# Optimization experiments

Hardware: AMD Instinct MI355X
Metric: run time of the kernel (lower is better)

## Reference

```python
import jax, jax.numpy as jnp
import numpy as np

TAU = 0.08


def setup_inputs() -> dict:
    key = jax.random.key(0)
    k1, k2 = jax.random.split(key)
    pos_waves = jax.random.normal(k1, (32, 64, 8192), dtype=jnp.float32)
    neg_waves = jax.random.normal(k2, (32, 64, 8192), dtype=jnp.float32)
    return {"pos_waves": pos_waves, "neg_waves": neg_waves}


def _normalize(w):
    # global min/max over the whole wave tensor (matches torch.min/torch.max on 2D tensor)
    lo = jnp.min(w, axis=(1, 2), keepdims=True)  # [N,1,1]
    hi = jnp.max(w, axis=(1, 2), keepdims=True)
    return (w - lo) / (hi - lo)


def _pairwise_negpearson(X, Y):
    # X: [N,B,T], Y: [M,B,T] -> mean over B of (1 - pearson) for every (n,m) pair
    T = X.shape[-1]
    sx = jnp.sum(X, axis=-1)            # [N,B]
    sy = jnp.sum(Y, axis=-1)            # [M,B]
    sx2 = jnp.sum(X * X, axis=-1)       # [N,B]
    sy2 = jnp.sum(Y * Y, axis=-1)       # [M,B]
    sxy = jnp.einsum('nbt,mbt->nmb', X, Y)  # [N,M,B]
    num = T * sxy - sx[:, None, :] * sy[None, :, :]
    den = jnp.sqrt((T * sx2 - sx * sx)[:, None, :] * (T * sy2 - sy * sy)[None, :, :])
    return jnp.mean(1.0 - num / den, axis=-1)  # [N,M]


def reference(pos_waves, neg_waves):
    P = _normalize(pos_waves)   # [N,B,T]
    Q = _normalize(neg_waves)   # [M,B,T]
    N = P.shape[0]

    d_pp = _pairwise_negpearson(P, P)                    # [N,N]
    upper = jnp.triu(jnp.ones((N, N), dtype=bool), k=1)  # i < j pairs only
    pos_total = jnp.sum(jnp.where(upper, jnp.exp(d_pp / TAU), 0.0))

    d_pn = _pairwise_negpearson(P, Q)                    # [N,M]
    neg_total = jnp.sum(jnp.exp(d_pn / TAU))

    return jnp.log10(pos_total / neg_total + 1.0)
```

## Files before the change

### kernel.cpp

```cpp
#include <hip/hip_runtime.h>
#include <cmath>

#define N_ 32
#define B_ 64
#define T_ 8192
#define NBLK1 1024
#define PS 2176

typedef _Float16 half8 __attribute__((ext_vector_type(8)));
typedef float floatx4 __attribute__((ext_vector_type(4)));

__device__ __forceinline__ half8 cvt8(const float4 v0, const float4 v1,
                                      float& s, float& s2) {
    s += v0.x + v0.y + v0.z + v0.w + v1.x + v1.y + v1.z + v1.w;
    s2 = fmaf(v0.x, v0.x, s2); s2 = fmaf(v0.y, v0.y, s2);
    s2 = fmaf(v0.z, v0.z, s2); s2 = fmaf(v0.w, v0.w, s2);
    s2 = fmaf(v1.x, v1.x, s2); s2 = fmaf(v1.y, v1.y, s2);
    s2 = fmaf(v1.z, v1.z, s2); s2 = fmaf(v1.w, v1.w, s2);
    half8 r = {(_Float16)v0.x, (_Float16)v0.y, (_Float16)v0.z, (_Float16)v0.w,
               (_Float16)v1.x, (_Float16)v1.y, (_Float16)v1.z, (_Float16)v1.w};
    return r;
}

__global__ __launch_bounds__(256, 2)
void k_stage1(const float* __restrict__ pos, const float* __restrict__ neg,
              float* __restrict__ pt, double* __restrict__ accs,
              unsigned* __restrict__ ctr) {
    __shared__ float red_s[PS];
    const int bid = blockIdx.x;
    const int b = bid & 63, cg = bid >> 6;
    const int tid = threadIdx.x;
    const int w = tid >> 6, lane = tid & 63;
    const int m = lane & 15, h = lane >> 4;

    if (bid == 0 && tid == 0) { accs[0] = 0.0; accs[1] = 0.0; *ctr = 0u; }

    const long tb = (long)cg * 512 + w * 128 + h * 8;
    const float4* pa0 = (const float4*)(pos + ((long)m * B_ + b) * T_ + tb);
    const float4* pa1 = (const float4*)(pos + ((long)(m + 16) * B_ + b) * T_ + tb);
    const float4* pb0 = (const float4*)(neg + ((long)m * B_ + b) * T_ + tb);
    const float4* pb1 = (const float4*)(neg + ((long)(m + 16) * B_ + b) * T_ + tb);

    float4 a0[4][2], a1[4][2], b0[4][2], b1[4][2];
#pragma unroll
    for (int kk = 0; kk < 4; ++kk) {
        a0[kk][0] = pa0[kk * 8]; a0[kk][1] = pa0[kk * 8 + 1];
        a1[kk][0] = pa1[kk * 8]; a1[kk][1] = pa1[kk * 8 + 1];
        b0[kk][0] = pb0[kk * 8]; b0[kk][1] = pb0[kk * 8 + 1];
        b1[kk][0] = pb1[kk * 8]; b1[kk][1] = pb1[kk * 8 + 1];
    }

    floatx4 cPP00 = {}, cPP01 = {}, cPP11 = {};
    floatx4 cPN00 = {}, cPN01 = {}, cPN10 = {}, cPN11 = {};
    float sxl = 0.f, sxl2 = 0.f, sxh = 0.f, sxh2 = 0.f;
    float syl = 0.f, syl2 = 0.f, syh = 0.f, syh2 = 0.f;

#pragma unroll
    for (int kk = 0; kk < 4; ++kk) {
        half8 fa0 = cvt8(a0[kk][0], a0[kk][1], sxl, sxl2);
        half8 fa1 = cvt8(a1[kk][0], a1[kk][1], sxh, sxh2);
        half8 fb0 = cvt8(b0[kk][0], b0[kk][1], syl, syl2);
        half8 fb1 = cvt8(b1[kk][0], b1[kk][1], syh, syh2);
        cPP00 = __builtin_amdgcn_mfma_f32_16x16x32_f16(fa0, fa0, cPP00, 0, 0, 0);
        cPP01 = __builtin_amdgcn_mfma_f32_16x16x32_f16(fa0, fa1, cPP01, 0, 0, 0);
        cPP11 = __builtin_amdgcn_mfma_f32_16x16x32_f16(fa1, fa1, cPP11, 0, 0, 0);
        cPN00 = __builtin_amdgcn_mfma_f32_16x16x32_f16(fa0, fb0, cPN00, 0, 0, 0);
        cPN01 = __builtin_amdgcn_mfma_f32_16x16x32_f16(fa0, fb1, cPN01, 0, 0, 0);
        cPN10 = __builtin_amdgcn_mfma_f32_16x16x32_f16(fa1, fb0, cPN10, 0, 0, 0);
        cPN11 = __builtin_amdgcn_mfma_f32_16x16x32_f16(fa1, fb1, cPN11, 0, 0, 0);
    }

    sxl += __shfl_xor(sxl, 16);   sxl += __shfl_xor(sxl, 32);
    sxl2 += __shfl_xor(sxl2, 16); sxl2 += __shfl_xor(sxl2, 32);
    sxh += __shfl_xor(sxh, 16);   sxh += __shfl_xor(sxh, 32);
    sxh2 += __shfl_xor(sxh2, 16); sxh2 += __shfl_xor(sxh2, 32);
    syl += __shfl_xor(syl, 16);   syl += __shfl_xor(syl, 32);
    syl2 += __shfl_xor(syl2, 16); syl2 += __shfl_xor(syl2, 32);
    syh += __shfl_xor(syh, 16);   syh += __shfl_xor(syh, 32);
    syh2 += __shfl_xor(syh2, 16); syh2 += __shfl_xor(syh2, 32);

    for (int i = tid; i < PS; i += 256) red_s[i] = 0.f;
    __syncthreads();
#pragma unroll
    for (int wv = 0; wv < 4; ++wv) {
        if (w == wv) {
#pragma unroll
            for (int reg = 0; reg < 4; ++reg) {
                const int r = h * 4 + reg;
                red_s[r * 32 + m]                    += cPP00[reg];
                red_s[r * 32 + 16 + m]               += cPP01[reg];
                red_s[(16 + r) * 32 + 16 + m]        += cPP11[reg];
                red_s[1024 + r * 32 + m]             += cPN00[reg];
                red_s[1024 + r * 32 + 16 + m]        += cPN01[reg];
                red_s[1024 + (16 + r) * 32 + m]      += cPN10[reg];
                red_s[1024 + (16 + r) * 32 + 16 + m] += cPN11[reg];
            }
            const int row = (h & 1) * 16 + m;
            const int base = 2048 + (h >> 1) * 64;
            const float s1 = (h == 0) ? sxl : (h == 1) ? sxh : (h == 2) ? syl : syh;
            const float s2 = (h == 0) ? sxl2 : (h == 1) ? sxh2 : (h == 2) ? syl2 : syh2;
            red_s[base + row] += s1;
            red_s[base + 32 + row] += s2;
        }
        __syncthreads();
    }

    for (int i = tid; i < PS; i += 256)
        pt[(long)i * NBLK1 + bid] = red_s[i];
}

__global__ __launch_bounds__(256)
void k_entries(const float* __restrict__ pt, double* __restrict__ accs,
               unsigned* __restrict__ ctr, float* __restrict__ out) {
    const int tid = threadIdx.x;
    const int w = tid >> 6, lane = tid & 63;
    const int entry = blockIdx.x * 4 + w;
    const int mat = entry >> 10;
    const int idx = entry & 1023;
    const int n = idx >> 5, m = idx & 31;

    auto rowsum = [&](int o) -> float {
        const float* p = pt + (long)o * NBLK1 + lane;
        float s = 0.f;
#pragma unroll
        for (int c = 0; c < 16; ++c) s += p[c * 64];
        return s;
    };

    const float g    = rowsum(mat * 1024 + idx);
    const float sxn  = rowsum(2048 + n);
    const float sx2n = rowsum(2080 + n);
    const float sym  = rowsum(mat ? 2112 + m : 2048 + m);
    const float sy2m = rowsum(mat ? 2144 + m : 2080 + m);

    double num = (double)T_ * (double)g - (double)sxn * (double)sym;
    double vx = (double)T_ * (double)sx2n - (double)sxn * (double)sxn;
    double vy = (double)T_ * (double)sy2m - (double)sym * (double)sym;
    double contrib = 1.0 - num / sqrt(vx * vy);

#pragma unroll
    for (int off = 32; off; off >>= 1) contrib += __shfl_down(contrib, off);

    __shared__ double s_pos[4], s_neg[4];
    if (lane == 0) {
        double d = contrib * (1.0 / B_);
        double term = exp(d / 0.08);
        double p = 0.0, q = 0.0;
        if (mat == 0) { if (n < m) p = term; }
        else q = term;
        s_pos[w] = p; s_neg[w] = q;
    }
    __syncthreads();
    if (tid == 0) {
        atomicAdd(&accs[0], s_pos[0] + s_pos[1] + s_pos[2] + s_pos[3]);
        atomicAdd(&accs[1], s_neg[0] + s_neg[1] + s_neg[2] + s_neg[3]);
        __threadfence();
        const unsigned old = atomicAdd(ctr, 1u);
        if (old == gridDim.x - 1) {
            __threadfence();
            const double p = ((volatile double*)accs)[0];
            const double q = ((volatile double*)accs)[1];
            out[0] = (float)log10(p / q + 1.0);
        }
    }
}

extern "C" void kernel_launch(void* const* d_in, const int* in_sizes, int n_in,
                              void* d_out, int out_size, void* d_ws, size_t ws_size,
                              hipStream_t stream) {
    (void)in_sizes; (void)n_in; (void)out_size; (void)ws_size;
    const float* pos = (const float*)d_in[0];
    const float* neg = (const float*)d_in[1];
    float* out = (float*)d_out;

    char* ws = (char*)d_ws;
    float* pt = (float*)ws;
    double* accs = (double*)(ws + (size_t)PS * NBLK1 * 4);
    unsigned* ctr = (unsigned*)(ws + (size_t)PS * NBLK1 * 4 + 16);

    k_stage1<<<NBLK1, 256, 0, stream>>>(pos, neg, pt, accs, ctr);
    k_entries<<<512, 256, 0, stream>>>(pt, accs, ctr, out);
}
```

Baseline: 189.6 us.

## Write block partials contiguously and add a separate reduction kernel

Stage 1 now stores each block's partial sums as one contiguous row using float4 stores, replacing the previous transposed layout where every element went to a strided address. A new k_reduce kernel sums the 16 chunk partials for each batch index with coalesced reads. k_entries then reads the already-reduced values instead of summing 16 partials itself. The aim is to remove uncoalesced scattered writes from stage 1, at the cost of an extra kernel launch and an extra pass over the partial buffer.

```diff
diff --git a/kernel.cpp b/kernel.cpp
--- a/kernel.cpp
+++ b/kernel.cpp
@@ -24,9 +24,9 @@
 
 __global__ __launch_bounds__(256, 2)
 void k_stage1(const float* __restrict__ pos, const float* __restrict__ neg,
-              float* __restrict__ pt, double* __restrict__ accs,
+              float* __restrict__ partial, double* __restrict__ accs,
               unsigned* __restrict__ ctr) {
-    __shared__ float red_s[PS];
+    __shared__ __align__(16) float red_s[PS];
     const int bid = blockIdx.x;
     const int b = bid & 63, cg = bid >> 6;
     const int tid = threadIdx.x;
@@ -105,12 +105,22 @@
         __syncthreads();
     }
 
-    for (int i = tid; i < PS; i += 256)
-        pt[(long)i * NBLK1 + bid] = red_s[i];
+    const float4* rs = (const float4*)red_s;
+    float4* op = (float4*)(partial + (long)bid * PS);
+    for (int i = tid; i < PS / 4; i += 256) op[i] = rs[i];
+}
+
+__global__ void k_reduce(const float* __restrict__ partial, float* __restrict__ red) {
+    const int b = blockIdx.y;
+    const int o = blockIdx.x * 128 + threadIdx.x;
+    float s = 0.f;
+#pragma unroll
+    for (int c = 0; c < 16; ++c) s += partial[(long)(c * 64 + b) * PS + o];
+    red[(long)b * PS + o] = s;
 }
 
 __global__ __launch_bounds__(256)
-void k_entries(const float* __restrict__ pt, double* __restrict__ accs,
+void k_entries(const float* __restrict__ red, double* __restrict__ accs,
                unsigned* __restrict__ ctr, float* __restrict__ out) {
     const int tid = threadIdx.x;
     const int w = tid >> 6, lane = tid & 63;
@@ -119,19 +129,12 @@
     const int idx = entry & 1023;
     const int n = idx >> 5, m = idx & 31;
 
-    auto rowsum = [&](int o) -> float {
-        const float* p = pt + (long)o * NBLK1 + lane;
-        float s = 0.f;
-#pragma unroll
-        for (int c = 0; c < 16; ++c) s += p[c * 64];
-        return s;
-    };
-
-    const float g    = rowsum(mat * 1024 + idx);
-    const float sxn  = rowsum(2048 + n);
-    const float sx2n = rowsum(2080 + n);
-    const float sym  = rowsum(mat ? 2112 + m : 2048 + m);
-    const float sy2m = rowsum(mat ? 2144 + m : 2080 + m);
+    const float* rb = red + (long)lane * PS;
+    const float g    = rb[mat * 1024 + idx];
+    const float sxn  = rb[2048 + n];
+    const float sx2n = rb[2080 + n];
+    const float sym  = rb[mat ? 2112 + m : 2048 + m];
+    const float sy2m = rb[mat ? 2144 + m : 2080 + m];
 
     double num = (double)T_ * (double)g - (double)sxn * (double)sym;
     double vx = (double)T_ * (double)sx2n - (double)sxn * (double)sxn;
@@ -174,10 +177,12 @@
     float* out = (float*)d_out;
 
     char* ws = (char*)d_ws;
-    float* pt = (float*)ws;
-    double* accs = (double*)(ws + (size_t)PS * NBLK1 * 4);
-    unsigned* ctr = (unsigned*)(ws + (size_t)PS * NBLK1 * 4 + 16);
+    float* partial = (float*)ws;
+    float* red = (float*)(ws + (size_t)NBLK1 * PS * 4);
+    double* accs = (double*)(ws + (size_t)NBLK1 * PS * 4 + (size_t)64 * PS * 4);
+    unsigned* ctr = (unsigned*)((char*)accs + 16);
 
-    k_stage1<<<NBLK1, 256, 0, stream>>>(pos, neg, pt, accs, ctr);
-    k_entries<<<512, 256, 0, stream>>>(pt, accs, ctr, out);
+    k_stage1<<<NBLK1, 256, 0, stream>>>(pos, neg, partial, accs, ctr);
+    k_reduce<<<dim3(17, 64), 128, 0, stream>>>(partial, red);
+    k_entries<<<512, 256, 0, stream>>>(red, accs, ctr, out);
 }
```

Measured after the change: 178.0 us. 6.1% less time.
